# Kernel optimization log

Hardware: AMD Instinct MI355X
Metric: run time of the kernel (lower is better)

The kernel has to match this reference:

```python
import jax, jax.numpy as jnp
import numpy as np

N = 100000          # nodes (src == target here)
E = 1600000         # edges, avg degree 16
C_IN = 128
C_OUT = 128
R = 7               # num_edge_types
T = 4               # num_node_types


def setup_inputs() -> dict:
    key = jax.random.key(0)
    ks = jax.random.split(key, 7)
    x = jax.random.normal(ks[0], (N, C_IN), dtype=jnp.float32)
    edge_index = jax.random.randint(ks[1], (2, E), 0, N, dtype=jnp.int32)
    edge_type = jax.random.randint(ks[2], (E,), 0, R, dtype=jnp.int32)
    target_node_type = jax.random.randint(ks[3], (N,), 0, T, dtype=jnp.int32)
    # Linear weights: rel_lins (no bias), root_lins (with bias); torch Linear: y = x @ W.T + b
    rel_w = jax.random.normal(ks[4], (R, C_OUT, C_IN), dtype=jnp.float32) * (1.0 / np.sqrt(C_IN))
    root_w = jax.random.normal(ks[5], (T, C_OUT, C_IN), dtype=jnp.float32) * (1.0 / np.sqrt(C_IN))
    root_b = jax.random.normal(ks[6], (T, C_OUT), dtype=jnp.float32) * 0.01
    return {"x": x, "edge_index": edge_index, "edge_type": edge_type,
            "target_node_type": target_node_type,
            "rel_w": rel_w, "root_w": root_w, "root_b": root_b}


def reference(x, edge_index, edge_type, target_node_type, rel_w, root_w, root_b):
    # Per-edge-type gather -> (bias-free) linear -> scatter-mean.
    # linear commutes with mean (no bias), so aggregate first, then apply W_r.
    n = x.shape[0]
    src, dst = edge_index[0], edge_index[1]
    x_j = x[src]                                   # [E, C_in] gather
    seg = dst.astype(jnp.int32) * R + edge_type    # fused (node, edge_type) segment id
    sums = jax.ops.segment_sum(x_j, seg, num_segments=n * R).reshape(n, R, C_IN)
    cnt = jax.ops.segment_sum(jnp.ones((x_j.shape[0],), x.dtype), seg,
                              num_segments=n * R).reshape(n, R)
    means = sums / jnp.maximum(cnt, 1.0)[:, :, None]   # zero rows stay zero (PyG mean of empty = 0)
    out = jnp.einsum('nrc,roc->no', means, rel_w)       # sum_r rel_lins[r](mean_r)
    # Per-node-type root linear with bias (small loop over T=4 types).
    for t in range(T):
        m = (target_node_type == t).astype(x.dtype)[:, None]
        out = out + m * (x @ root_w[t].T + root_b[t])
    return out
```

## Files before the change

kernel.cpp:

```cpp
#include <hip/hip_runtime.h>

#define N_NODES 100000
#define N_EDGES 1600000
#define C_DIM   128
#define R_TYPES 7
#define T_TYPES 4
#define SEGS    (N_NODES * R_TYPES)
#define NB_E    (N_EDGES / 256)
#define NB_N    ((N_NODES + 255) / 256)
#define XP_ROWS 100096
#define DST_PART 12500

#define OFF_CNTI   0ull
#define OFF_INV    2800000ull
#define OFF_DOFF   5600000ull
#define OFF_CURS   6000004ull
#define OFF_MISC   6400004ull
#define OFF_PERM   6400132ull
#define PERM_CAP   100288
#define N_PERM_BLOCKS 1567
#define OFF_BLKN   6801284ull
#define OFF_BSUM   6813796ull
#define OFF_ESRC   6815360ull
#define OFF_XP     13215360ull
#define OFF_WF     38839936ull
#define OFF_XWB    39069312ull
#define XWB_PLANE  ((size_t)XP_ROWS * 128)
#define FULL_NEED  218441344ull
#define FB_NEED    64693888ull
#define OFF_WRF    OFF_CNTI

typedef __attribute__((ext_vector_type(8))) short short8;
typedef __attribute__((ext_vector_type(4))) float f32x4;

__device__ inline unsigned short f2bf(float f) {
    unsigned int u = __float_as_uint(f);
    u += 0x7fffu + ((u >> 16) & 1u);
    return (unsigned short)(u >> 16);
}
__device__ inline float bf2f(unsigned int h) { return __uint_as_float(h << 16); }

__global__ void edge_hist(const int* __restrict__ ei, const int* __restrict__ et,
                          int* __restrict__ cnti) {
    int e = blockIdx.x * 256 + threadIdx.x;
    atomicAdd(&cnti[ei[N_EDGES + e] * R_TYPES + et[e]], 1);
}

__global__ void inv_kernel(const int* __restrict__ cnti, float* __restrict__ inv) {
    int i = blockIdx.x * blockDim.x + threadIdx.x;
    if (i < SEGS) inv[i] = 1.0f / (float)max(cnti[i], 1);
}

__global__ void dst_scan1(const int* __restrict__ cnti, int* __restrict__ dst_off,
                          int* __restrict__ bsum) {
    __shared__ int sbuf[256];
    int tid = threadIdx.x;
    int i = blockIdx.x * 256 + tid;
    int v = 0;
    if (i < N_NODES) {
        #pragma unroll
        for (int r = 0; r < R_TYPES; ++r) v += cnti[i * R_TYPES + r];
    }
    sbuf[tid] = v;
    __syncthreads();
    #pragma unroll
    for (int off = 1; off < 256; off <<= 1) {
        int t = (tid >= off) ? sbuf[tid - off] : 0;
        __syncthreads();
        sbuf[tid] += t;
        __syncthreads();
    }
    int incl = sbuf[tid];
    if (i < N_NODES) dst_off[i] = incl - v;
    if (tid == 255) bsum[blockIdx.x] = incl;
}

__global__ void seg_scan2(int* __restrict__ bsum, int nb) {
    __shared__ int sbuf[256];
    int tid = threadIdx.x;
    int running = 0;
    for (int c0 = 0; c0 < nb; c0 += 256) {
        int b = c0 + tid;
        int v = (b < nb) ? bsum[b] : 0;
        sbuf[tid] = v;
        __syncthreads();
        #pragma unroll
        for (int off = 1; off < 256; off <<= 1) {
            int t = (tid >= off) ? sbuf[tid - off] : 0;
            __syncthreads();
            sbuf[tid] += t;
            __syncthreads();
        }
        int incl = sbuf[tid];
        int tot = sbuf[255];
        __syncthreads();
        if (b < nb) bsum[b] = running + incl - v;
        running += tot;
    }
}

__global__ void dst_scan3(int* __restrict__ dst_off, int* __restrict__ cursor,
                          const int* __restrict__ bsum) {
    int i = blockIdx.x * 256 + threadIdx.x;
    if (i < N_NODES) {
        int val = dst_off[i] + bsum[blockIdx.x];
        dst_off[i] = val;
        cursor[i] = val;
    }
    if (i == 0) dst_off[N_NODES] = N_EDGES;
}

__global__ void place_edges(const int* __restrict__ ei, const int* __restrict__ et,
                            int* __restrict__ cursor, int* __restrict__ esrc) {
    int p = blockIdx.x & 7;
    int e = (blockIdx.x >> 3) * 256 + threadIdx.x;
    int d = ei[N_EDGES + e];
    if (d / DST_PART != p) return;
    int pos = atomicAdd(&cursor[d], 1);
    int r = et[e];
    esrc[pos] = (r << 20) | (r * XP_ROWS + ei[e]);
}

__global__ void node_hist(const int* __restrict__ tnt, int* __restrict__ blk_n) {
    __shared__ int h[8];
    int tid = threadIdx.x;
    if (tid < 8) h[tid] = 0;
    __syncthreads();
    int n = blockIdx.x * 256 + tid;
    if (n < N_NODES) atomicAdd(&h[tnt[n]], 1);
    __syncthreads();
    if (tid < T_TYPES) blk_n[blockIdx.x * 8 + tid] = h[tid];
}

__global__ void scan_blocks(int* __restrict__ blk, int nb, int* __restrict__ total) {
    __shared__ int sbuf[256];
    int r = blockIdx.x;
    int tid = threadIdx.x;
    int running = 0;
    for (int c0 = 0; c0 < nb; c0 += 256) {
        int b = c0 + tid;
        int v = (b < nb) ? blk[b * 8 + r] : 0;
        sbuf[tid] = v;
        __syncthreads();
        #pragma unroll
        for (int off = 1; off < 256; off <<= 1) {
            int t = (tid >= off) ? sbuf[tid - off] : 0;
            __syncthreads();
            sbuf[tid] += t;
            __syncthreads();
        }
        int incl = sbuf[tid];
        int chunk_total = sbuf[255];
        __syncthreads();
        if (b < nb) blk[b * 8 + r] = running + incl - v;
        running += chunk_total;
    }
    if (tid == 0) total[r] = running;
}

__global__ void offsets_kernel(int* misc) {
    if (threadIdx.x == 0 && blockIdx.x == 0) {
        int s = 0;
        for (int t = 0; t < T_TYPES; ++t) {
            misc[4 + t] = s;
            s += ((misc[t] + 63) / 64) * 64;
        }
    }
}

__global__ void node_scatter(const int* __restrict__ tnt, const int* __restrict__ misc,
                             const int* __restrict__ blk_n, int* __restrict__ perm) {
    __shared__ int h[8];
    int tid = threadIdx.x;
    if (tid < 8) h[tid] = 0;
    __syncthreads();
    int n = blockIdx.x * 256 + tid;
    if (n < N_NODES) {
        int t = tnt[n];
        int rank = atomicAdd(&h[t], 1);
        perm[misc[4 + t] + blk_n[blockIdx.x * 8 + t] + rank] = n;
    }
}

__global__ void cvt_x_frag(const float* __restrict__ x, unsigned short* __restrict__ xp) {
    int id = blockIdx.x * 256 + threadIdx.x;
    int n = id >> 4, ko = id & 15;
    short8 o;
    if (n < N_NODES) {
        const float4* px = (const float4*)(x + (size_t)n * C_DIM + ko * 8);
        float4 a = px[0], b = px[1];
        o[0] = (short)f2bf(a.x); o[1] = (short)f2bf(a.y);
        o[2] = (short)f2bf(a.z); o[3] = (short)f2bf(a.w);
        o[4] = (short)f2bf(b.x); o[5] = (short)f2bf(b.y);
        o[6] = (short)f2bf(b.z); o[7] = (short)f2bf(b.w);
    } else {
        o = (short8)0;
    }
    size_t off = (size_t)(n >> 4) * 2048 + (ko >> 2) * 512 + (ko & 3) * 128 + (n & 15) * 8;
    *(short8*)(xp + off) = o;
}

__global__ void cvt_w_frag(const float* __restrict__ rel_w, unsigned short* __restrict__ wf) {
    int id = blockIdx.x * 256 + threadIdx.x;
    if (id >= R_TYPES * 128 * 16) return;
    int r = id >> 11, rest = id & 2047;
    int o = rest >> 4, ko = rest & 15;
    const float4* pw = (const float4*)(rel_w + (size_t)r * 16384 + o * 128 + ko * 8);
    float4 a = pw[0], b = pw[1];
    short8 v;
    v[0] = (short)f2bf(a.x); v[1] = (short)f2bf(a.y);
    v[2] = (short)f2bf(a.z); v[3] = (short)f2bf(a.w);
    v[4] = (short)f2bf(b.x); v[5] = (short)f2bf(b.y);
    v[6] = (short)f2bf(b.z); v[7] = (short)f2bf(b.w);
    size_t off = (size_t)r * 16384 + (o >> 4) * 2048 + (ko >> 2) * 512 + (ko & 3) * 128 + (o & 15) * 8;
    *(short8*)(wf + off) = v;
}

__global__ void cvt_rootw_frag(const float* __restrict__ root_w, unsigned short* __restrict__ wrf) {
    int id = blockIdx.x * 256 + threadIdx.x;
    if (id >= T_TYPES * 128 * 16) return;
    int t = id >> 11, rest = id & 2047;
    int o = rest >> 4, ko = rest & 15;
    const float4* pw = (const float4*)(root_w + (size_t)t * 16384 + o * 128 + ko * 8);
    float4 a = pw[0], b = pw[1];
    float v[8] = {a.x, a.y, a.z, a.w, b.x, b.y, b.z, b.w};
    short8 hi, lo;
    #pragma unroll
    for (int j = 0; j < 8; ++j) {
        unsigned short h = f2bf(v[j]);
        hi[j] = (short)h;
        lo[j] = (short)f2bf(v[j] - bf2f(h));
    }
    size_t off = (size_t)t * 16384 + (o >> 4) * 2048 + (ko >> 2) * 512 + (ko & 3) * 128 + (o & 15) * 8;
    *(short8*)(wrf + off) = hi;
    *(short8*)(wrf + (size_t)T_TYPES * 16384 + off) = lo;
}

__launch_bounds__(256)
__global__ void xw_gemm_all(const unsigned short* __restrict__ xp,
                            const unsigned short* __restrict__ wf,
                            unsigned short* __restrict__ xwb7) {
    int wave = threadIdx.x >> 6, lane = threadIdx.x & 63;
    int m0 = blockIdx.x * 128;

    short8 a[4][2];
    #pragma unroll
    for (int kb = 0; kb < 4; ++kb)
        #pragma unroll
        for (int rt = 0; rt < 2; ++rt) {
            size_t rtile = (size_t)blockIdx.x * 8 + wave * 2 + rt;
            a[kb][rt] = *(const short8*)(xp + rtile * 2048 + kb * 512 + lane * 8);
        }

    int col = lane & 15, rq = (lane >> 4) * 4;
    for (int r = 0; r < R_TYPES; ++r) {
        const unsigned short* wr = wf + (size_t)r * 16384;
        unsigned short* xwb = xwb7 + (size_t)r * XWB_PLANE;
        #pragma unroll
        for (int ct = 0; ct < 8; ++ct) {
            f32x4 acc0 = (f32x4)0.0f, acc1 = (f32x4)0.0f;
            #pragma unroll
            for (int kb = 0; kb < 4; ++kb) {
                short8 b = *(const short8*)(wr + (size_t)ct * 2048 + kb * 512 + lane * 8);
                acc0 = __builtin_amdgcn_mfma_f32_16x16x32_bf16(a[kb][0], b, acc0, 0, 0, 0);
                acc1 = __builtin_amdgcn_mfma_f32_16x16x32_bf16(a[kb][1], b, acc1, 0, 0, 0);
            }
            #pragma unroll
            for (int i = 0; i < 4; ++i) {
                int n0 = m0 + wave * 32 + rq + i;
                if (n0 < N_NODES)
                    xwb[(size_t)n0 * C_DIM + ct * 16 + col] = f2bf(acc0[i]);
                int n1 = n0 + 16;
                if (n1 < N_NODES)
                    xwb[(size_t)n1 * C_DIM + ct * 16 + col] = f2bf(acc1[i]);
            }
        }
    }
}

__launch_bounds__(256)
__global__ void xw_gemm_mfma(const unsigned short* __restrict__ xp,
                             const unsigned short* __restrict__ wf,
                             unsigned short* __restrict__ xwb, int r) {
    int wave = threadIdx.x >> 6, lane = threadIdx.x & 63;
    int m0 = blockIdx.x * 128;
    const unsigned short* wr = wf + (size_t)r * 16384;

    short8 a[4][2];
    #pragma unroll
    for (int kb = 0; kb < 4; ++kb)
        #pragma unroll
        for (int rt = 0; rt < 2; ++rt) {
            size_t rtile = (size_t)blockIdx.x * 8 + wave * 2 + rt;
            a[kb][rt] = *(const short8*)(xp + rtile * 2048 + kb * 512 + lane * 8);
        }

    int col = lane & 15, rq = (lane >> 4) * 4;
    #pragma unroll
    for (int ct = 0; ct < 8; ++ct) {
        f32x4 acc0 = (f32x4)0.0f, acc1 = (f32x4)0.0f;
        #pragma unroll
        for (int kb = 0; kb < 4; ++kb) {
            short8 b = *(const short8*)(wr + (size_t)ct * 2048 + kb * 512 + lane * 8);
            acc0 = __builtin_amdgcn_mfma_f32_16x16x32_bf16(a[kb][0], b, acc0, 0, 0, 0);
            acc1 = __builtin_amdgcn_mfma_f32_16x16x32_bf16(a[kb][1], b, acc1, 0, 0, 0);
        }
        #pragma unroll
        for (int i = 0; i < 4; ++i) {
            int n0 = m0 + wave * 32 + rq + i;
            if (n0 < N_NODES)
                xwb[(size_t)n0 * C_DIM + ct * 16 + col] = f2bf(acc0[i]);
            int n1 = n0 + 16;
            if (n1 < N_NODES)
                xwb[(size_t)n1 * C_DIM + ct * 16 + col] = f2bf(acc1[i]);
        }
    }
}

__global__ void gather_fused(const int* __restrict__ dst_off, const int* __restrict__ esrc,
                             const float* __restrict__ inv,
                             const unsigned short* __restrict__ xwb7,
                             float* __restrict__ out) {
    int wave = threadIdx.x >> 6, lane = threadIdx.x & 63;
    int d = blockIdx.x * 4 + wave;
    if (d >= N_NODES) return;
    int o0 = dst_off[d], o1 = dst_off[d + 1];
    int q = lane >> 4;
    int l16 = lane & 15;
    const float* invd = inv + d * R_TYPES;
    float acc[8];
    #pragma unroll
    for (int j = 0; j < 8; ++j) acc[j] = 0.f;

    int e = o0;
    int pkA = 0, pkB = 0;
    bool run = (e + 8 <= o1);
    if (run) { pkA = esrc[e + q]; pkB = esrc[e + 4 + q]; }
    while (run) {
        uint4 rA = *(const uint4*)(xwb7 + (size_t)(pkA & 0xFFFFF) * C_DIM + l16 * 8);
        uint4 rB = *(const uint4*)(xwb7 + (size_t)(pkB & 0xFFFFF) * C_DIM + l16 * 8);
        float sA = invd[pkA >> 20];
        float sB = invd[pkB >> 20];
        e += 8;
        run = (e + 8 <= o1);
        if (run) { pkA = esrc[e + q]; pkB = esrc[e + 4 + q]; }
        acc[0] += bf2f(rA.x & 0xffffu) * sA;  acc[1] += bf2f(rA.x >> 16) * sA;
        acc[2] += bf2f(rA.y & 0xffffu) * sA;  acc[3] += bf2f(rA.y >> 16) * sA;
        acc[4] += bf2f(rA.z & 0xffffu) * sA;  acc[5] += bf2f(rA.z >> 16) * sA;
        acc[6] += bf2f(rA.w & 0xffffu) * sA;  acc[7] += bf2f(rA.w >> 16) * sA;
        acc[0] += bf2f(rB.x & 0xffffu) * sB;  acc[1] += bf2f(rB.x >> 16) * sB;
        acc[2] += bf2f(rB.y & 0xffffu) * sB;  acc[3] += bf2f(rB.y >> 16) * sB;
        acc[4] += bf2f(rB.z & 0xffffu) * sB;  acc[5] += bf2f(rB.z >> 16) * sB;
        acc[6] += bf2f(rB.w & 0xffffu) * sB;  acc[7] += bf2f(rB.w >> 16) * sB;
    }
    for (; e < o1; e += 4) {
        int idx = e + q;
        bool valid = idx < o1;
        int pk = esrc[valid ? idx : e];
        uint4 rw = *(const uint4*)(xwb7 + (size_t)(pk & 0xFFFFF) * C_DIM + l16 * 8);
        float s = valid ? invd[pk >> 20] : 0.0f;
        acc[0] += bf2f(rw.x & 0xffffu) * s;  acc[1] += bf2f(rw.x >> 16) * s;
        acc[2] += bf2f(rw.y & 0xffffu) * s;  acc[3] += bf2f(rw.y >> 16) * s;
        acc[4] += bf2f(rw.z & 0xffffu) * s;  acc[5] += bf2f(rw.z >> 16) * s;
        acc[6] += bf2f(rw.w & 0xffffu) * s;  acc[7] += bf2f(rw.w >> 16) * s;
    }

    #pragma unroll
    for (int j = 0; j < 8; ++j) {
        acc[j] += __shfl_xor(acc[j], 16);
        acc[j] += __shfl_xor(acc[j], 32);
    }
    if (lane < 16) {
        float4* po = (float4*)(out + (size_t)d * C_DIM + l16 * 8);
        po[0] = make_float4(acc[0], acc[1], acc[2], acc[3]);
        po[1] = make_float4(acc[4], acc[5], acc[6], acc[7]);
    }
}

__global__ void gather_rel_f(const int* __restrict__ dst_off, const int* __restrict__ esrc,
                             const float* __restrict__ inv,
                             const unsigned short* __restrict__ xwb,
                             float* __restrict__ out, int rf) {
    int wave = threadIdx.x >> 6, lane = threadIdx.x & 63;
    int d = blockIdx.x * 4 + wave;
    if (d >= N_NODES) return;
    int o0 = dst_off[d], o1 = dst_off[d + 1];
    float ax = 0.0f, ay = 0.0f;
    bool any = false;
    for (int e = o0; e < o1; ++e) {
        int pk = esrc[e];
        if ((pk >> 20) != rf) continue;
        any = true;
        int src = (pk & 0xFFFFF) - rf * XP_ROWS;
        unsigned int row = *(const unsigned int*)(xwb + (size_t)src * C_DIM + lane * 2);
        ax += bf2f(row & 0xffffu);
        ay += bf2f(row >> 16);
    }
    if (!any) return;
    float sc = inv[d * R_TYPES + rf];
    float2* po = (float2*)(out + (size_t)d * C_DIM) + lane;
    float2 v = *po;
    v.x += ax * sc;
    v.y += ay * sc;
    *po = v;
}

__launch_bounds__(256)
__global__ void root_mfma(const float* __restrict__ x, const unsigned short* __restrict__ wrf,
                          const float* __restrict__ root_b, const int* __restrict__ tnt,
                          const int* __restrict__ perm, float* __restrict__ out) {
    __shared__ int pidx[64];
    int tid = threadIdx.x;
    int wave = tid >> 6, lane = tid & 63;
    if (tid < 64) pidx[tid] = perm[blockIdx.x * 64 + tid];
    __syncthreads();
    if (pidx[0] < 0) return;
    int t = tnt[pidx[0]];

    int node = pidx[wave * 16 + (lane & 15)];
    int k0 = (lane >> 4) * 8;
    short8 ah[4], al[4];
    #pragma unroll
    for (int kb = 0; kb < 4; ++kb) {
        float v[8];
        if (node >= 0) {
            const float4* px = (const float4*)(x + (size_t)node * C_DIM + kb * 32 + k0);
            float4 p0 = px[0], p1 = px[1];
            v[0] = p0.x; v[1] = p0.y; v[2] = p0.z; v[3] = p0.w;
            v[4] = p1.x; v[5] = p1.y; v[6] = p1.z; v[7] = p1.w;
        } else {
            #pragma unroll
            for (int j = 0; j < 8; ++j) v[j] = 0.0f;
        }
        #pragma unroll
        for (int j = 0; j < 8; ++j) {
            unsigned short h = f2bf(v[j]);
            ah[kb][j] = (short)h;
            al[kb][j] = (short)f2bf(v[j] - bf2f(h));
        }
    }

    const unsigned short* wh = wrf + (size_t)t * 16384;
    const unsigned short* wl = wrf + (size_t)(T_TYPES + t) * 16384;
    int col = lane & 15, rq = (lane >> 4) * 4;
    #pragma unroll
    for (int ct = 0; ct < 8; ++ct) {
        f32x4 acc = (f32x4)0.0f;
        #pragma unroll
        for (int kb = 0; kb < 4; ++kb) {
            short8 bh = *(const short8*)(wh + ct * 2048 + kb * 512 + lane * 8);
            short8 bl = *(const short8*)(wl + ct * 2048 + kb * 512 + lane * 8);
            acc = __builtin_amdgcn_mfma_f32_16x16x32_bf16(ah[kb], bh, acc, 0, 0, 0);
            acc = __builtin_amdgcn_mfma_f32_16x16x32_bf16(al[kb], bh, acc, 0, 0, 0);
            acc = __builtin_amdgcn_mfma_f32_16x16x32_bf16(ah[kb], bl, acc, 0, 0, 0);
        }
        float bias = root_b[t * 128 + ct * 16 + col];
        #pragma unroll
        for (int i = 0; i < 4; ++i) {
            int nr = pidx[wave * 16 + rq + i];
            if (nr >= 0) {
                float* po = out + (size_t)nr * C_DIM + ct * 16 + col;
                *po += acc[i] + bias;
            }
        }
    }
}

extern "C" void kernel_launch(void* const* d_in, const int* in_sizes, int n_in,
                              void* d_out, int out_size, void* d_ws, size_t ws_size,
                              hipStream_t stream) {
    const float* x      = (const float*)d_in[0];
    const int*   ei     = (const int*)d_in[1];
    const int*   et     = (const int*)d_in[2];
    const int*   tnt    = (const int*)d_in[3];
    const float* rel_w  = (const float*)d_in[4];
    const float* root_w = (const float*)d_in[5];
    const float* root_b = (const float*)d_in[6];
    float* out = (float*)d_out;

    char* ws = (char*)d_ws;
    int*   cnti    = (int*)(ws + OFF_CNTI);
    float* inv     = (float*)(ws + OFF_INV);
    int*   dst_off = (int*)(ws + OFF_DOFF);
    int*   cursor  = (int*)(ws + OFF_CURS);
    int*   misc    = (int*)(ws + OFF_MISC);
    int*   perm    = (int*)(ws + OFF_PERM);
    int*   blk_n   = (int*)(ws + OFF_BLKN);
    int*   bsum    = (int*)(ws + OFF_BSUM);
    int*   esrc    = (int*)(ws + OFF_ESRC);
    unsigned short* xp  = (unsigned short*)(ws + OFF_XP);
    unsigned short* wf  = (unsigned short*)(ws + OFF_WF);
    unsigned short* xwb = (unsigned short*)(ws + OFF_XWB);
    unsigned short* wrf = (unsigned short*)(ws + OFF_WRF);

    const bool full = (ws_size >= FULL_NEED);

    hipMemsetAsync(ws + OFF_CNTI, 0, SEGS * sizeof(int), stream);
    hipMemsetAsync(ws + OFF_MISC, 0, 32 * sizeof(int), stream);
    hipMemsetAsync(ws + OFF_PERM, 0xFF, (size_t)PERM_CAP * sizeof(int), stream);
    if (!full)
        hipMemsetAsync(d_out, 0, (size_t)out_size * sizeof(float), stream);

    edge_hist  <<<NB_E, 256, 0, stream>>>(ei, et, cnti);
    inv_kernel <<<(SEGS + 255) / 256, 256, 0, stream>>>(cnti, inv);
    dst_scan1  <<<NB_N, 256, 0, stream>>>(cnti, dst_off, bsum);
    seg_scan2  <<<1, 256, 0, stream>>>(bsum, NB_N);
    dst_scan3  <<<NB_N, 256, 0, stream>>>(dst_off, cursor, bsum);
    place_edges<<<NB_E * 8, 256, 0, stream>>>(ei, et, cursor, esrc);

    cvt_rootw_frag<<<32, 256, 0, stream>>>(root_w, wrf);

    node_hist  <<<NB_N, 256, 0, stream>>>(tnt, blk_n);
    scan_blocks<<<T_TYPES, 256, 0, stream>>>(blk_n, NB_N, misc + 0);
    offsets_kernel<<<1, 64, 0, stream>>>(misc);
    node_scatter<<<NB_N, 256, 0, stream>>>(tnt, misc, blk_n, perm);

    cvt_x_frag<<<(XP_ROWS * 16) / 256, 256, 0, stream>>>(x, xp);
    cvt_w_frag<<<56, 256, 0, stream>>>(rel_w, wf);

    if (full) {
        xw_gemm_all <<<XP_ROWS / 128, 256, 0, stream>>>(xp, wf, xwb);
        gather_fused<<<(N_NODES + 3) / 4, 256, 0, stream>>>(dst_off, esrc, inv, xwb, out);
    } else {
        for (int r = 0; r < R_TYPES; ++r) {
            xw_gemm_mfma<<<XP_ROWS / 128, 256, 0, stream>>>(xp, wf, xwb, r);
            gather_rel_f<<<(N_NODES + 3) / 4, 256, 0, stream>>>(dst_off, esrc, inv, xwb, out, r);
        }
    }
    root_mfma<<<N_PERM_BLOCKS, 256, 0, stream>>>(x, wrf, root_b, tnt, perm, out);
}
```

Baseline: 494.1 us.

## Compute root linear first with block-local type grouping, fold into gather

Replaces the global node-type permutation pipeline (histogram, scan, offsets, scatter) with a root kernel that groups each 64-node block by type in shared memory. That root kernel now runs first and writes its result to out directly. The fused gather kernel then loads the prior out row and adds the aggregated messages, so the separate output memset and the read-modify-write root pass are no longer needed. This cuts several small launches and one full pass over out. In exchange, each block may run partly empty 16-row tiles, and the non-full fallback path (gather_rel_f) may now rely on out holding the root result rather than zero.

Measured after the change: 470.3 us. -4.8%, faster.

```diff
diff --git a/kernel.cpp b/kernel.cpp
--- a/kernel.cpp
+++ b/kernel.cpp
@@ -10,6 +10,7 @@
 #define NB_N    ((N_NODES + 255) / 256)
 #define XP_ROWS 100096
 #define DST_PART 12500
+#define NB_ROOT ((N_NODES + 63) / 64)
 
 #define OFF_CNTI   0ull
 #define OFF_INV    2800000ull
@@ -18,7 +19,6 @@
 #define OFF_MISC   6400004ull
 #define OFF_PERM   6400132ull
 #define PERM_CAP   100288
-#define N_PERM_BLOCKS 1567
 #define OFF_BLKN   6801284ull
 #define OFF_BSUM   6813796ull
 #define OFF_ESRC   6815360ull
@@ -28,7 +28,7 @@
 #define XWB_PLANE  ((size_t)XP_ROWS * 128)
 #define FULL_NEED  218441344ull
 #define FB_NEED    64693888ull
-#define OFF_WRF    OFF_CNTI
+#define OFF_WRF    OFF_PERM
 
 typedef __attribute__((ext_vector_type(8))) short short8;
 typedef __attribute__((ext_vector_type(4))) float f32x4;
@@ -119,67 +119,6 @@
     int pos = atomicAdd(&cursor[d], 1);
     int r = et[e];
     esrc[pos] = (r << 20) | (r * XP_ROWS + ei[e]);
-}
-
-__global__ void node_hist(const int* __restrict__ tnt, int* __restrict__ blk_n) {
-    __shared__ int h[8];
-    int tid = threadIdx.x;
-    if (tid < 8) h[tid] = 0;
-    __syncthreads();
-    int n = blockIdx.x * 256 + tid;
-    if (n < N_NODES) atomicAdd(&h[tnt[n]], 1);
-    __syncthreads();
-    if (tid < T_TYPES) blk_n[blockIdx.x * 8 + tid] = h[tid];
-}
-
-__global__ void scan_blocks(int* __restrict__ blk, int nb, int* __restrict__ total) {
-    __shared__ int sbuf[256];
-    int r = blockIdx.x;
-    int tid = threadIdx.x;
-    int running = 0;
-    for (int c0 = 0; c0 < nb; c0 += 256) {
-        int b = c0 + tid;
-        int v = (b < nb) ? blk[b * 8 + r] : 0;
-        sbuf[tid] = v;
-        __syncthreads();
-        #pragma unroll
-        for (int off = 1; off < 256; off <<= 1) {
-            int t = (tid >= off) ? sbuf[tid - off] : 0;
-            __syncthreads();
-            sbuf[tid] += t;
-            __syncthreads();
-        }
-        int incl = sbuf[tid];
-        int chunk_total = sbuf[255];
-        __syncthreads();
-        if (b < nb) blk[b * 8 + r] = running + incl - v;
-        running += chunk_total;
-    }
-    if (tid == 0) total[r] = running;
-}
-
-__global__ void offsets_kernel(int* misc) {
-    if (threadIdx.x == 0 && blockIdx.x == 0) {
-        int s = 0;
-        for (int t = 0; t < T_TYPES; ++t) {
-            misc[4 + t] = s;
-            s += ((misc[t] + 63) / 64) * 64;
-        }
-    }
-}
-
-__global__ void node_scatter(const int* __restrict__ tnt, const int* __restrict__ misc,
-                             const int* __restrict__ blk_n, int* __restrict__ perm) {
-    __shared__ int h[8];
-    int tid = threadIdx.x;
-    if (tid < 8) h[tid] = 0;
-    __syncthreads();
-    int n = blockIdx.x * 256 + tid;
-    if (n < N_NODES) {
-        int t = tnt[n];
-        int rank = atomicAdd(&h[t], 1);
-        perm[misc[4 + t] + blk_n[blockIdx.x * 8 + t] + rank] = n;
-    }
 }
 
 __global__ void cvt_x_frag(const float* __restrict__ x, unsigned short* __restrict__ xp) {
@@ -237,6 +176,91 @@
 }
 
 __launch_bounds__(256)
+__global__ void root_nat(const float* __restrict__ x, const unsigned short* __restrict__ wrf,
+                         const float* __restrict__ root_b, const int* __restrict__ tnt,
+                         float* __restrict__ out) {
+    __shared__ int cnt[T_TYPES];
+    __shared__ int goff[T_TYPES];
+    __shared__ int rankb[64];
+    __shared__ int lidx[112];
+    __shared__ int ttyp[8];
+    __shared__ int ntile_s;
+    int tid = threadIdx.x;
+    int base = blockIdx.x * 64;
+    if (tid < T_TYPES) cnt[tid] = 0;
+    if (tid < 112) lidx[tid] = -1;
+    __syncthreads();
+    int myt = -1;
+    if (tid < 64 && base + tid < N_NODES) {
+        myt = tnt[base + tid];
+        rankb[tid] = atomicAdd(&cnt[myt], 1);
+    }
+    __syncthreads();
+    if (tid == 0) {
+        int s = 0;
+        for (int t = 0; t < T_TYPES; ++t) {
+            goff[t] = s;
+            int nt = (cnt[t] + 15) >> 4;
+            for (int k = 0; k < nt; ++k) ttyp[(s >> 4) + k] = t;
+            s += nt << 4;
+        }
+        ntile_s = s >> 4;
+    }
+    __syncthreads();
+    if (myt >= 0) lidx[goff[myt] + rankb[tid]] = base + tid;
+    __syncthreads();
+    int ntiles = ntile_s;
+
+    int wave = tid >> 6, lane = tid & 63;
+    int l16 = lane & 15, kq = lane >> 4;
+    for (int tile = wave; tile < ntiles; tile += 4) {
+        int t = ttyp[tile];
+        int node = lidx[tile * 16 + l16];
+        short8 ah[4], al[4];
+        #pragma unroll
+        for (int kb = 0; kb < 4; ++kb) {
+            float v[8];
+            if (node >= 0) {
+                const float4* px = (const float4*)(x + (size_t)node * C_DIM + kb * 32 + kq * 8);
+                float4 p0 = px[0], p1 = px[1];
+                v[0] = p0.x; v[1] = p0.y; v[2] = p0.z; v[3] = p0.w;
+                v[4] = p1.x; v[5] = p1.y; v[6] = p1.z; v[7] = p1.w;
+            } else {
+                #pragma unroll
+                for (int j = 0; j < 8; ++j) v[j] = 0.0f;
+            }
+            #pragma unroll
+            for (int j = 0; j < 8; ++j) {
+                unsigned short h = f2bf(v[j]);
+                ah[kb][j] = (short)h;
+                al[kb][j] = (short)f2bf(v[j] - bf2f(h));
+            }
+        }
+        const unsigned short* wh = wrf + (size_t)t * 16384;
+        const unsigned short* wl = wh + (size_t)T_TYPES * 16384;
+        #pragma unroll
+        for (int ct = 0; ct < 8; ++ct) {
+            f32x4 acc = (f32x4)0.0f;
+            #pragma unroll
+            for (int kb = 0; kb < 4; ++kb) {
+                short8 bh = *(const short8*)(wh + ct * 2048 + kb * 512 + lane * 8);
+                short8 bl = *(const short8*)(wl + ct * 2048 + kb * 512 + lane * 8);
+                acc = __builtin_amdgcn_mfma_f32_16x16x32_bf16(ah[kb], bh, acc, 0, 0, 0);
+                acc = __builtin_amdgcn_mfma_f32_16x16x32_bf16(al[kb], bh, acc, 0, 0, 0);
+                acc = __builtin_amdgcn_mfma_f32_16x16x32_bf16(ah[kb], bl, acc, 0, 0, 0);
+            }
+            float bias = root_b[t * 128 + ct * 16 + l16];
+            #pragma unroll
+            for (int i = 0; i < 4; ++i) {
+                int nr = lidx[tile * 16 + kq * 4 + i];
+                if (nr >= 0)
+                    out[(size_t)nr * C_DIM + ct * 16 + l16] = acc[i] + bias;
+            }
+        }
+    }
+}
+
+__launch_bounds__(256)
 __global__ void xw_gemm_all(const unsigned short* __restrict__ xp,
                             const unsigned short* __restrict__ wf,
                             unsigned short* __restrict__ xwb7) {
@@ -328,6 +352,11 @@
     int q = lane >> 4;
     int l16 = lane & 15;
     const float* invd = inv + d * R_TYPES;
+
+    float4 prev = make_float4(0.f, 0.f, 0.f, 0.f);
+    int fidx = (l16 << 1) | q;
+    if (lane < 32) prev = ((const float4*)(out + (size_t)d * C_DIM))[fidx];
+
     float acc[8];
     #pragma unroll
     for (int j = 0; j < 8; ++j) acc[j] = 0.f;
@@ -370,10 +399,13 @@
         acc[j] += __shfl_xor(acc[j], 16);
         acc[j] += __shfl_xor(acc[j], 32);
     }
-    if (lane < 16) {
-        float4* po = (float4*)(out + (size_t)d * C_DIM + l16 * 8);
-        po[0] = make_float4(acc[0], acc[1], acc[2], acc[3]);
-        po[1] = make_float4(acc[4], acc[5], acc[6], acc[7]);
+    if (lane < 32) {
+        float4 w;
+        if (lane < 16)
+            w = make_float4(acc[0] + prev.x, acc[1] + prev.y, acc[2] + prev.z, acc[3] + prev.w);
+        else
+            w = make_float4(acc[4] + prev.x, acc[5] + prev.y, acc[6] + prev.z, acc[7] + prev.w);
+        ((float4*)(out + (size_t)d * C_DIM))[fidx] = w;
     }
 }
 
@@ -405,67 +437,6 @@
     *po = v;
 }
 
-__launch_bounds__(256)
-__global__ void root_mfma(const float* __restrict__ x, const unsigned short* __restrict__ wrf,
-                          const float* __restrict__ root_b, const int* __restrict__ tnt,
-                          const int* __restrict__ perm, float* __restrict__ out) {
-    __shared__ int pidx[64];
-    int tid = threadIdx.x;
-    int wave = tid >> 6, lane = tid & 63;
-    if (tid < 64) pidx[tid] = perm[blockIdx.x * 64 + tid];
-    __syncthreads();
-    if (pidx[0] < 0) return;
-    int t = tnt[pidx[0]];
-
-    int node = pidx[wave * 16 + (lane & 15)];
-    int k0 = (lane >> 4) * 8;
-    short8 ah[4], al[4];
-    #pragma unroll
-    for (int kb = 0; kb < 4; ++kb) {
-        float v[8];
-        if (node >= 0) {
-            const float4* px = (const float4*)(x + (size_t)node * C_DIM + kb * 32 + k0);
-            float4 p0 = px[0], p1 = px[1];
-            v[0] = p0.x; v[1] = p0.y; v[2] = p0.z; v[3] = p0.w;
-            v[4] = p1.x; v[5] = p1.y; v[6] = p1.z; v[7] = p1.w;
-        } else {
-            #pragma unroll
-            for (int j = 0; j < 8; ++j) v[j] = 0.0f;
-        }
-        #pragma unroll
-        for (int j = 0; j < 8; ++j) {
-            unsigned short h = f2bf(v[j]);
-            ah[kb][j] = (short)h;
-            al[kb][j] = (short)f2bf(v[j] - bf2f(h));
-        }
-    }
-
-    const unsigned short* wh = wrf + (size_t)t * 16384;
-    const unsigned short* wl = wrf + (size_t)(T_TYPES + t) * 16384;
-    int col = lane & 15, rq = (lane >> 4) * 4;
-    #pragma unroll
-    for (int ct = 0; ct < 8; ++ct) {
-        f32x4 acc = (f32x4)0.0f;
-        #pragma unroll
-        for (int kb = 0; kb < 4; ++kb) {
-            short8 bh = *(const short8*)(wh + ct * 2048 + kb * 512 + lane * 8);
-            short8 bl = *(const short8*)(wl + ct * 2048 + kb * 512 + lane * 8);
-            acc = __builtin_amdgcn_mfma_f32_16x16x32_bf16(ah[kb], bh, acc, 0, 0, 0);
-            acc = __builtin_amdgcn_mfma_f32_16x16x32_bf16(al[kb], bh, acc, 0, 0, 0);
-            acc = __builtin_amdgcn_mfma_f32_16x16x32_bf16(ah[kb], bl, acc, 0, 0, 0);
-        }
-        float bias = root_b[t * 128 + ct * 16 + col];
-        #pragma unroll
-        for (int i = 0; i < 4; ++i) {
-            int nr = pidx[wave * 16 + rq + i];
-            if (nr >= 0) {
-                float* po = out + (size_t)nr * C_DIM + ct * 16 + col;
-                *po += acc[i] + bias;
-            }
-        }
-    }
-}
-
 extern "C" void kernel_launch(void* const* d_in, const int* in_sizes, int n_in,
                               void* d_out, int out_size, void* d_ws, size_t ws_size,
                               hipStream_t stream) {
@@ -483,9 +454,6 @@
     float* inv     = (float*)(ws + OFF_INV);
     int*   dst_off = (int*)(ws + OFF_DOFF);
     int*   cursor  = (int*)(ws + OFF_CURS);
-    int*   misc    = (int*)(ws + OFF_MISC);
-    int*   perm    = (int*)(ws + OFF_PERM);
-    int*   blk_n   = (int*)(ws + OFF_BLKN);
     int*   bsum    = (int*)(ws + OFF_BSUM);
     int*   esrc    = (int*)(ws + OFF_ESRC);
     unsigned short* xp  = (unsigned short*)(ws + OFF_XP);
@@ -496,10 +464,9 @@
     const bool full = (ws_size >= FULL_NEED);
 
     hipMemsetAsync(ws + OFF_CNTI, 0, SEGS * sizeof(int), stream);
-    hipMemsetAsync(ws + OFF_MISC, 0, 32 * sizeof(int), stream);
-    hipMemsetAsync(ws + OFF_PERM, 0xFF, (size_t)PERM_CAP * sizeof(int), stream);
-    if (!full)
-        hipMemsetAsync(d_out, 0, (size_t)out_size * sizeof(float), stream);
+
+    cvt_rootw_frag<<<32, 256, 0, stream>>>(root_w, wrf);
+    root_nat<<<NB_ROOT, 256, 0, stream>>>(x, wrf, root_b, tnt, out);
 
     edge_hist  <<<NB_E, 256, 0, stream>>>(ei, et, cnti);
     inv_kernel <<<(SEGS + 255) / 256, 256, 0, stream>>>(cnti, inv);
@@ -507,13 +474,6 @@
     seg_scan2  <<<1, 256, 0, stream>>>(bsum, NB_N);
     dst_scan3  <<<NB_N, 256, 0, stream>>>(dst_off, cursor, bsum);
     place_edges<<<NB_E * 8, 256, 0, stream>>>(ei, et, cursor, esrc);
-
-    cvt_rootw_frag<<<32, 256, 0, stream>>>(root_w, wrf);
-
-    node_hist  <<<NB_N, 256, 0, stream>>>(tnt, blk_n);
-    scan_blocks<<<T_TYPES, 256, 0, stream>>>(blk_n, NB_N, misc + 0);
-    offsets_kernel<<<1, 64, 0, stream>>>(misc);
-    node_scatter<<<NB_N, 256, 0, stream>>>(tnt, misc, blk_n, perm);
 
     cvt_x_frag<<<(XP_ROWS * 16) / 256, 256, 0, stream>>>(x, xp);
     cvt_w_frag<<<56, 256, 0, stream>>>(rel_w, wf);
@@ -527,5 +487,4 @@
             gather_rel_f<<<(N_NODES + 3) / 4, 256, 0, stream>>>(dst_off, esrc, inv, xwb, out, r);
         }
     }
-    root_mfma<<<N_PERM_BLOCKS, 256, 0, stream>>>(x, wrf, root_b, tnt, perm, out);
-}
+}
```
